# Kernel tuning notes

Measured on AMD Instinct MI355X. Metric: run time of the kernel, lower is better.

## Reference

```python
import jax, jax.numpy as jnp
import numpy as np

N, L, S, D, H = 4, 8192, 8192, 256, 8
DH = D // H  # 32
EPS_ATTN = 1e-6
EPS_LN = 1e-5


def setup_inputs() -> dict:
    key = jax.random.key(0)
    ks = jax.random.split(key, 8)
    w = lambda k, sh: jax.random.normal(k, sh, jnp.float32) * 0.02
    return {
        "x": jax.random.normal(ks[0], (N, L, D), jnp.float32),
        "source": jax.random.normal(ks[1], (N, S, D), jnp.float32),
        "Wq": w(ks[2], (D, D)),
        "Wk": w(ks[3], (D, D)),
        "Wv": w(ks[4], (D, D)),
        "Wm": w(ks[5], (D, D)),
        "W1": w(ks[6], (2 * D, 2 * D)),
        "W2": w(ks[7], (2 * D, D)),
        "g1": jnp.ones((D,), jnp.float32),
        "b1": jnp.zeros((D,), jnp.float32),
        "g2": jnp.ones((D,), jnp.float32),
        "b2": jnp.zeros((D,), jnp.float32),
    }


def _layernorm(x, g, b):
    m = jnp.mean(x, axis=-1, keepdims=True)
    v = jnp.var(x, axis=-1, keepdims=True)
    return (x - m) * jax.lax.rsqrt(v + EPS_LN) * g + b


def reference(x, source, Wq, Wk, Wv, Wm, W1, W2, g1, b1, g2, b2):
    bs = x.shape[0]
    # QKV projections (bias=False), split heads -> [N, L/S, H, DH]
    q = (x @ Wq).reshape(bs, -1, H, DH)
    k = (source @ Wk).reshape(bs, -1, H, DH)
    v = (source @ Wv).reshape(bs, -1, H, DH)
    # elu+1 feature map (linear attention, LoFTR-style)
    Q = jax.nn.elu(q) + 1.0
    K = jax.nn.elu(k) + 1.0
    v_len = v.shape[1]
    vals = v / v_len
    KV = jnp.einsum("nshd,nshv->nhdv", K, vals)  # [N, H, DH, DH]
    Z = 1.0 / (jnp.einsum("nlhd,nhd->nlh", Q, K.sum(axis=1)) + EPS_ATTN)
    msg = jnp.einsum("nlhd,nhdv,nlh->nlhv", Q, KV, Z) * v_len  # [N, L, H, DH]
    # merge heads + LN
    msg = msg.reshape(bs, -1, H * DH) @ Wm
    msg = _layernorm(msg, g1, b1)
    # concat-MLP with LeakyReLU(0.1)
    h = jnp.concatenate([x, msg], axis=2) @ W1
    h = jnp.where(h >= 0, h, 0.1 * h)
    msg = h @ W2
    msg = _layernorm(msg, g2, b2)
    return x + msg
```

## Files before the change

kernel.cpp:

```cpp
#include <hip/hip_runtime.h>

typedef __bf16 bf16;
typedef __bf16 bf16x4 __attribute__((ext_vector_type(4)));
typedef __bf16 bf16x8 __attribute__((ext_vector_type(8)));
typedef float f32x4 __attribute__((ext_vector_type(4)));

#define BM 128
#define BN 128
#define BK 64

__device__ __forceinline__ float apply_epi(float v, int epi) {
  if (epi == 1) return v > 0.f ? v + 1.f : __expf(v);
  if (epi == 2) return v >= 0.f ? v : 0.1f * v;
  return v;
}

__device__ __forceinline__ void g2l16(const bf16* gp, bf16* lp) {
  __builtin_amdgcn_global_load_lds(
      (const __attribute__((address_space(1))) void*)gp,
      (__attribute__((address_space(3))) void*)lp, 16, 0, 0);
}

__global__ void detect_kernel(const unsigned* g1raw, int* flag) {
  if (threadIdx.x == 0 && blockIdx.x == 0)
    *flag = (g1raw[0] == 0x3F800000u) ? 1 : 0;
}

struct TransArgs {
  const void* src[6];
  bf16* dst[6];
  int R[6], C[6], t0[6];
};

__global__ __launch_bounds__(256) void prep_kernel(
    const void* __restrict__ xin, const void* __restrict__ sin,
    bf16* __restrict__ bx, bf16* __restrict__ bs,
    TransArgs ta, const int* flagp) {
  const bool f32 = (*flagp != 0);
  if (blockIdx.x < 8192) {
    const void* s;
    bf16* d;
    size_t i;
    if (blockIdx.x < 4096) {
      s = xin; d = bx; i = (size_t)blockIdx.x * 2048 + threadIdx.x * 8;
    } else {
      s = sin; d = bs; i = (size_t)(blockIdx.x - 4096) * 2048 + threadIdx.x * 8;
    }
    if (f32) {
      f32x4 lo = *(const f32x4*)((const float*)s + i);
      f32x4 hi = *(const f32x4*)((const float*)s + i + 4);
      bf16x8 t;
      t[0] = (bf16)lo[0]; t[1] = (bf16)lo[1]; t[2] = (bf16)lo[2]; t[3] = (bf16)lo[3];
      t[4] = (bf16)hi[0]; t[5] = (bf16)hi[1]; t[6] = (bf16)hi[2]; t[7] = (bf16)hi[3];
      *(bf16x8*)(d + i) = t;
    } else {
      *(bf16x8*)(d + i) = *(const bf16x8*)((const bf16*)s + i);
    }
    return;
  }
  __shared__ bf16 tile[32][33];
  int bid = blockIdx.x - 8192;
  int si = 0;
#pragma unroll
  for (int i = 1; i < 6; ++i)
    if (bid >= ta.t0[i]) si = i;
  const void* srcv = ta.src[si];
  bf16* dst = ta.dst[si];
  int R = ta.R[si], Cc = ta.C[si];
  int lt = bid - ta.t0[si];
  int tpr = Cc >> 5;
  int tr = lt / tpr, tc = lt % tpr;
  int tx = threadIdx.x & 31, ty0 = threadIdx.x >> 5;
#pragma unroll
  for (int i = 0; i < 4; ++i) {
    int ty = ty0 + i * 8;
    size_t idx = (size_t)(tr * 32 + ty) * Cc + tc * 32 + tx;
    tile[ty][tx] = f32 ? (bf16)((const float*)srcv)[idx] : ((const bf16*)srcv)[idx];
  }
  __syncthreads();
#pragma unroll
  for (int i = 0; i < 4; ++i) {
    int ty = ty0 + i * 8;
    dst[(size_t)(tc * 32 + ty) * R + tr * 32 + tx] = tile[tx][ty];
  }
}

__global__ __launch_bounds__(256) void gemm_rt(
    const bf16* __restrict__ A, const bf16* __restrict__ A2, int ldA,
    const bf16* __restrict__ Bt, bf16* __restrict__ C, int Nn, int Kk, int epi,
    bf16* __restrict__ C2, int epi2, int split) {
  __shared__ bf16 As[BM * BK];
  __shared__ bf16 Bs[BN * BK];
  const int tid = threadIdx.x;
  const int m0 = blockIdx.x * BM;
  const int n0 = blockIdx.y * BN;
  const int wave = tid >> 6, lane = tid & 63;
  const int wm = (wave & 1) * 64, wn = (wave >> 1) * 64;
  const int q = lane >> 4, mr = lane & 15;

  f32x4 acc[4][4];
#pragma unroll
  for (int i = 0; i < 4; ++i)
#pragma unroll
    for (int j = 0; j < 4; ++j) acc[i][j] = (f32x4){0.f, 0.f, 0.f, 0.f};

  const int kTiles = Kk / BK;
  for (int kt = 0; kt < kTiles; ++kt) {
    int kk = kt * BK;
    const bf16* Ab = A;
    int kcol = kk;
    if (A2 && kk >= 256) { Ab = A2; kcol = kk - 256; }
    __syncthreads();
#pragma unroll
    for (int it = 0; it < 4; ++it) {
      int id = it * 256 + tid;
      int rr = id >> 3, pp = id & 7, gg = pp ^ (rr & 7);
      g2l16(Ab + (size_t)(m0 + rr) * ldA + kcol + gg * 8, &As[id * 8]);
    }
#pragma unroll
    for (int it = 0; it < 4; ++it) {
      int id = it * 256 + tid;
      int rr = id >> 3, pp = id & 7, gg = pp ^ (rr & 7);
      g2l16(Bt + (size_t)(n0 + rr) * Kk + kk + gg * 8, &Bs[id * 8]);
    }
    __syncthreads();
#pragma unroll
    for (int ks = 0; ks < 2; ++ks) {
      bf16x8 af[4], bfv[4];
#pragma unroll
      for (int mi = 0; mi < 4; ++mi) {
        int rrow = wm + mi * 16 + mr;
        af[mi] = *(const bf16x8*)&As[rrow * BK + ((ks * 4 + q) ^ (rrow & 7)) * 8];
      }
#pragma unroll
      for (int ni = 0; ni < 4; ++ni) {
        int rrow = wn + ni * 16 + mr;
        bfv[ni] = *(const bf16x8*)&Bs[rrow * BK + ((ks * 4 + q) ^ (rrow & 7)) * 8];
      }
#pragma unroll
      for (int mi = 0; mi < 4; ++mi)
#pragma unroll
        for (int ni = 0; ni < 4; ++ni)
          acc[mi][ni] = __builtin_amdgcn_mfma_f32_16x16x32_bf16(af[mi], bfv[ni], acc[mi][ni], 0, 0, 0);
    }
  }

  bf16* Cw = C;
  int nbase = n0, ep = epi;
  if (C2 && n0 >= split) { Cw = C2; nbase = n0 - split; ep = epi2; }
#pragma unroll
  for (int mi = 0; mi < 4; ++mi)
#pragma unroll
    for (int ni = 0; ni < 4; ++ni)
#pragma unroll
      for (int r4 = 0; r4 < 4; ++r4) {
        int row = m0 + wm + mi * 16 + q * 4 + r4;
        int cn = nbase + wn + ni * 16 + mr;
        float v = apply_epi(acc[mi][ni][r4], ep);
        Cw[(size_t)row * Nn + cn] = (bf16)v;
      }
}

#define KVCH 256
__global__ __launch_bounds__(256) void kv_kernel(
    const bf16* __restrict__ Kf, const bf16* __restrict__ V,
    float* __restrict__ partial, float* __restrict__ pk) {
  __shared__ bf16 Ks[KVCH][32];
  __shared__ bf16 Vs[KVCH][32];
  const int cb = blockIdx.x, h = blockIdx.y, n = blockIdx.z;
  const int tid = threadIdx.x;
  const int wave = tid >> 6, lane = tid & 63;
  const int d0 = (lane & 7) * 4, dv0 = (lane >> 3) * 4;
  const int s0 = cb * KVCH;
#pragma unroll
  for (int rd = 0; rd < 4; ++rd) {
    int rr = rd * 64 + (tid >> 2), pp = tid & 3;
    size_t g = ((size_t)(n * 8192 + s0 + rr)) * 256 + h * 32 + pp * 8;
    *(bf16x8*)&Ks[rr][pp * 8] = *(const bf16x8*)(Kf + g);
    *(bf16x8*)&Vs[rr][pp * 8] = *(const bf16x8*)(V + g);
  }
  __syncthreads();
  float acc[4][4] = {};
  float ks4[4] = {};
#pragma unroll 4
  for (int si = 0; si < 64; ++si) {
    int s = wave * 64 + si;
    bf16x4 k4 = *(const bf16x4*)&Ks[s][d0];
    bf16x4 v4 = *(const bf16x4*)&Vs[s][dv0];
    float kf[4] = {(float)k4[0], (float)k4[1], (float)k4[2], (float)k4[3]};
    float vf[4] = {(float)v4[0], (float)v4[1], (float)v4[2], (float)v4[3]};
#pragma unroll
    for (int vi = 0; vi < 4; ++vi)
#pragma unroll
      for (int di = 0; di < 4; ++di) acc[vi][di] = fmaf(vf[vi], kf[di], acc[vi][di]);
#pragma unroll
    for (int di = 0; di < 4; ++di) ks4[di] += kf[di];
  }
  __syncthreads();
  float* red = (float*)&Ks[0][0];
  float* ksr = (float*)&Vs[0][0];
#pragma unroll
  for (int vi = 0; vi < 4; ++vi)
#pragma unroll
    for (int di = 0; di < 4; ++di)
      red[wave * 1024 + (dv0 + vi) * 32 + d0 + di] = acc[vi][di];
  if (dv0 == 0) {
#pragma unroll
    for (int di = 0; di < 4; ++di) ksr[wave * 32 + d0 + di] = ks4[di];
  }
  __syncthreads();
  const size_t slot = (size_t)(n * 8 + h) * 32 + cb;
  f32x4 s4 = {0.f, 0.f, 0.f, 0.f};
#pragma unroll
  for (int w = 0; w < 4; ++w) s4 += *(const f32x4*)&red[w * 1024 + tid * 4];
  *(f32x4*)&partial[slot * 1024 + tid * 4] = s4;
  if (tid < 32) {
    float ss = 0.f;
#pragma unroll
    for (int w = 0; w < 4; ++w) ss += ksr[w * 32 + tid];
    pk[slot * 32 + tid] = ss;
  }
}

__global__ __launch_bounds__(256) void kv_reduce(
    const float* __restrict__ partial, const float* __restrict__ pk,
    float* __restrict__ kv_acc, float* __restrict__ ksum) {
  const int b = blockIdx.x;
  const int t = threadIdx.x;
  f32x4 s4 = {0.f, 0.f, 0.f, 0.f};
  for (int c = 0; c < 32; ++c)
    s4 += *(const f32x4*)&partial[((size_t)b * 32 + c) * 1024 + t * 4];
  *(f32x4*)&kv_acc[(size_t)b * 1024 + t * 4] = s4;
  if (t < 32) {
    float ss = 0.f;
    for (int c = 0; c < 32; ++c) ss += pk[((size_t)b * 32 + c) * 32 + t];
    ksum[(size_t)b * 32 + t] = ss;
  }
}

__global__ __launch_bounds__(256) void msg_kernel(
    const bf16* __restrict__ Q, const float* __restrict__ kv_acc,
    const float* __restrict__ ksum, bf16* __restrict__ msg) {
  __shared__ bf16 kvt[8][32][32];
  __shared__ float ksl[8][32];
  __shared__ float zl[8][128];
  int tid = threadIdx.x;
  int row0 = blockIdx.x * 128;
  int n = row0 >> 13;
  const float* kvb = kv_acc + (size_t)n * 8192;
  for (int i = tid; i < 8192; i += 256) ((bf16*)kvt)[i] = (bf16)kvb[i];
  ((float*)ksl)[tid] = ksum[(size_t)n * 256 + tid];
  __syncthreads();
  int r = tid & 127, hg = tid >> 7;
  const bf16* qrow = Q + (size_t)(row0 + r) * 256;
#pragma unroll
  for (int hh = 0; hh < 4; ++hh) {
    int h = hg * 4 + hh;
    float dot = 0.f;
#pragma unroll
    for (int d = 0; d < 32; ++d) dot = fmaf((float)qrow[h * 32 + d], ksl[h][d], dot);
    zl[h][r] = 1.f / (dot + 1e-6f);
  }
  __syncthreads();
  int wave = tid >> 6, lane = tid & 63, q = lane >> 4, mr = lane & 15;
  f32x4 zero = {0.f, 0.f, 0.f, 0.f};
  for (int h = 0; h < 8; ++h) {
    bf16x8 b0 = *(const bf16x8*)&kvt[h][mr][q * 8];
    bf16x8 b1 = *(const bf16x8*)&kvt[h][16 + mr][q * 8];
#pragma unroll
    for (int mi = 0; mi < 2; ++mi) {
      int arow = wave * 32 + mi * 16 + mr;
      bf16x8 a = *(const bf16x8*)(Q + (size_t)(row0 + arow) * 256 + h * 32 + q * 8);
      f32x4 c0 = __builtin_amdgcn_mfma_f32_16x16x32_bf16(a, b0, zero, 0, 0, 0);
      f32x4 c1 = __builtin_amdgcn_mfma_f32_16x16x32_bf16(a, b1, zero, 0, 0, 0);
#pragma unroll
      for (int r4 = 0; r4 < 4; ++r4) {
        int orow = wave * 32 + mi * 16 + q * 4 + r4;
        float z = zl[h][orow];
        size_t ob = (size_t)(row0 + orow) * 256 + h * 32;
        msg[ob + mr] = (bf16)(c0[r4] * z);
        msg[ob + 16 + mr] = (bf16)(c1[r4] * z);
      }
    }
  }
}

__global__ __launch_bounds__(256) void ln_kernel(
    const bf16* __restrict__ in, const void* __restrict__ g, const void* __restrict__ b,
    const void* __restrict__ resid, void* __restrict__ outp,
    const int* flagp, int ioDual) {
  const bool gbF32 = (*flagp != 0);
  const bool ioF32 = ioDual && gbF32;
  int wave = threadIdx.x >> 6, lane = threadIdx.x & 63;
  size_t row = (size_t)blockIdx.x * 4 + wave;
  int c = lane * 4;
  bf16x4 v = *(const bf16x4*)(in + row * 256 + c);
  float x0 = (float)v[0], x1 = (float)v[1], x2 = (float)v[2], x3 = (float)v[3];
  float s = x0 + x1 + x2 + x3;
  float sq = x0 * x0 + x1 * x1 + x2 * x2 + x3 * x3;
#pragma unroll
  for (int o = 32; o > 0; o >>= 1) {
    s += __shfl_xor(s, o);
    sq += __shfl_xor(sq, o);
  }
  float mean = s * (1.f / 256.f);
  float var = sq * (1.f / 256.f) - mean * mean;
  float rstd = rsqrtf(var + 1e-5f);
  float g0, g1v, g2v, g3, b0, b1v, b2v, b3;
  if (gbF32) {
    f32x4 gv = *(const f32x4*)((const float*)g + c);
    f32x4 bv = *(const f32x4*)((const float*)b + c);
    g0 = gv[0]; g1v = gv[1]; g2v = gv[2]; g3 = gv[3];
    b0 = bv[0]; b1v = bv[1]; b2v = bv[2]; b3 = bv[3];
  } else {
    bf16x4 gv = *(const bf16x4*)((const bf16*)g + c);
    bf16x4 bv = *(const bf16x4*)((const bf16*)b + c);
    g0 = (float)gv[0]; g1v = (float)gv[1]; g2v = (float)gv[2]; g3 = (float)gv[3];
    b0 = (float)bv[0]; b1v = (float)bv[1]; b2v = (float)bv[2]; b3 = (float)bv[3];
  }
  float y0 = (x0 - mean) * rstd * g0 + b0;
  float y1 = (x1 - mean) * rstd * g1v + b1v;
  float y2 = (x2 - mean) * rstd * g2v + b2v;
  float y3 = (x3 - mean) * rstd * g3 + b3;
  if (resid) {
    if (ioF32) {
      f32x4 rv = *(const f32x4*)((const float*)resid + row * 256 + c);
      y0 += rv[0]; y1 += rv[1]; y2 += rv[2]; y3 += rv[3];
    } else {
      bf16x4 rv = *(const bf16x4*)((const bf16*)resid + row * 256 + c);
      y0 += (float)rv[0]; y1 += (float)rv[1]; y2 += (float)rv[2]; y3 += (float)rv[3];
    }
  }
  if (ioF32) {
    f32x4 o4 = {y0, y1, y2, y3};
    *(f32x4*)((float*)outp + row * 256 + c) = o4;
  } else {
    bf16x4 o4;
    o4[0] = (bf16)y0; o4[1] = (bf16)y1; o4[2] = (bf16)y2; o4[3] = (bf16)y3;
    *(bf16x4*)((bf16*)outp + row * 256 + c) = o4;
  }
}

extern "C" void kernel_launch(void* const* d_in, const int* in_sizes, int n_in,
                              void* d_out, int out_size, void* d_ws, size_t ws_size,
                              hipStream_t stream) {
  const void* x   = d_in[0];
  const void* src = d_in[1];
  const void* Wq  = d_in[2];
  const void* Wk  = d_in[3];
  const void* Wv  = d_in[4];
  const void* Wm  = d_in[5];
  const void* W1  = d_in[6];
  const void* W2  = d_in[7];
  const void* g1  = d_in[8];
  const void* b1  = d_in[9];
  const void* g2  = d_in[10];
  const void* b2  = d_in[11];

  char* ws = (char*)d_ws;
  bf16* bufA = (bf16*)(ws);
  bf16* bufB = (bf16*)(ws + ((size_t)16 << 20));
  bf16* bufC = (bf16*)(ws + ((size_t)32 << 20));
  bf16* WqT  = (bf16*)(ws + ((size_t)48 << 20));
  bf16* WkvT = WqT + 65536;
  bf16* WmT  = WkvT + 131072;
  bf16* W1T  = WmT + 65536;
  bf16* W2T  = W1T + 262144;
  float* kv_acc = (float*)(ws + ((size_t)50 << 20));
  float* ksum = kv_acc + 32768;
  int* flagp = (int*)(ws + ((size_t)50 << 20) + 160 * 1024);
  float* partial = (float*)(ws + ((size_t)51 << 20));
  float* pk = (float*)(ws + ((size_t)55 << 20));
  bf16* bufX = (bf16*)d_out;
  bf16* bufS = bufX + 8388608;

  detect_kernel<<<dim3(1), dim3(64), 0, stream>>>((const unsigned*)g1, flagp);

  TransArgs ta;
  ta.src[0] = Wq; ta.src[1] = Wk; ta.src[2] = Wv; ta.src[3] = Wm; ta.src[4] = W1; ta.src[5] = W2;
  ta.dst[0] = WqT; ta.dst[1] = WkvT; ta.dst[2] = WkvT + 65536; ta.dst[3] = WmT; ta.dst[4] = W1T; ta.dst[5] = W2T;
  ta.R[0] = 256; ta.R[1] = 256; ta.R[2] = 256; ta.R[3] = 256; ta.R[4] = 512; ta.R[5] = 512;
  ta.C[0] = 256; ta.C[1] = 256; ta.C[2] = 256; ta.C[3] = 256; ta.C[4] = 512; ta.C[5] = 256;
  ta.t0[0] = 0; ta.t0[1] = 64; ta.t0[2] = 128; ta.t0[3] = 192; ta.t0[4] = 256; ta.t0[5] = 512;
  prep_kernel<<<dim3(8832), dim3(256), 0, stream>>>(x, src, bufX, bufS, ta, flagp);

  gemm_rt<<<dim3(256, 2), dim3(256), 0, stream>>>(bufX, nullptr, 256, WqT, bufA, 256, 256, 1,
                                                  nullptr, 0, 0);
  gemm_rt<<<dim3(256, 4), dim3(256), 0, stream>>>(bufS, nullptr, 256, WkvT, bufB, 256, 256, 1,
                                                  bufC, 0, 256);

  kv_kernel<<<dim3(32, 8, 4), dim3(256), 0, stream>>>(bufB, bufC, partial, pk);
  kv_reduce<<<dim3(32), dim3(256), 0, stream>>>(partial, pk, kv_acc, ksum);

  msg_kernel<<<dim3(256), dim3(256), 0, stream>>>(bufA, kv_acc, ksum, bufB);

  gemm_rt<<<dim3(256, 2), dim3(256), 0, stream>>>(bufB, nullptr, 256, WmT, bufA, 256, 256, 0,
                                                  nullptr, 0, 0);

  ln_kernel<<<dim3(8192), dim3(256), 0, stream>>>(bufA, g1, b1, nullptr, bufC, flagp, 0);

  gemm_rt<<<dim3(256, 4), dim3(256), 0, stream>>>(bufX, bufC, 256, W1T, bufA, 512, 512, 2,
                                                  nullptr, 0, 0);

  gemm_rt<<<dim3(256, 2), dim3(256), 0, stream>>>(bufA, nullptr, 512, W2T, bufC, 256, 512, 0,
                                                  nullptr, 0, 0);

  ln_kernel<<<dim3(8192), dim3(256), 0, stream>>>(bufC, g2, b2, x, d_out, flagp, 1);
}
```

Measured before the change: 284.4 us.

## Replace GEMM with double-buffered 256x256 tile kernel and swizzled block order

The 128x128 single-buffered GEMM becomes a 256x256-tile kernel with 512 threads and double-buffered LDS. The next K tile is prefetched while MFMA runs on the current one, and a block-index swizzle changes how tiles are assigned. This is meant to hide global-load latency and raise data reuse per block. In exchange the grids shrink to 128 or 256 workgroups, so occupancy on the GPU drops. The larger register footprint (32 accumulators per lane) could cause spills, and LDS use per block grows to 128 KB.

Result: slower. 293.4 us (+3.2%).

```diff
diff --git a/kernel.cpp b/kernel.cpp
--- a/kernel.cpp
+++ b/kernel.cpp
@@ -4,10 +4,6 @@
 typedef __bf16 bf16x4 __attribute__((ext_vector_type(4)));
 typedef __bf16 bf16x8 __attribute__((ext_vector_type(8)));
 typedef float f32x4 __attribute__((ext_vector_type(4)));
-
-#define BM 128
-#define BN 128
-#define BK 64
 
 __device__ __forceinline__ float apply_epi(float v, int epi) {
   if (epi == 1) return v > 0.f ? v + 1.f : __expf(v);
@@ -85,71 +81,97 @@
   }
 }
 
-__global__ __launch_bounds__(256) void gemm_rt(
+#define TM 256
+#define TN 256
+#define TK 64
+
+__device__ __forceinline__ void stage_tile(
+    const bf16* __restrict__ Ab, int ldA, int m0, int kcol,
+    const bf16* __restrict__ Bt, int Kk, int n0, int kk,
+    bf16* As, bf16* Bs, int tid) {
+#pragma unroll
+  for (int it = 0; it < 4; ++it) {
+    int id = it * 512 + tid;
+    int rr = id >> 3, pp = id & 7, gg = pp ^ (rr & 7);
+    g2l16(Ab + (size_t)(m0 + rr) * ldA + kcol + gg * 8, As + id * 8);
+  }
+#pragma unroll
+  for (int it = 0; it < 4; ++it) {
+    int id = it * 512 + tid;
+    int rr = id >> 3, pp = id & 7, gg = pp ^ (rr & 7);
+    g2l16(Bt + (size_t)(n0 + rr) * Kk + kk + gg * 8, Bs + id * 8);
+  }
+}
+
+__global__ __launch_bounds__(512, 2) void gemm256(
     const bf16* __restrict__ A, const bf16* __restrict__ A2, int ldA,
     const bf16* __restrict__ Bt, bf16* __restrict__ C, int Nn, int Kk, int epi,
-    bf16* __restrict__ C2, int epi2, int split) {
-  __shared__ bf16 As[BM * BK];
-  __shared__ bf16 Bs[BN * BK];
+    bf16* __restrict__ C2, int epi2, int split, int gridM) {
+  __shared__ bf16 As[2][TM * TK];
+  __shared__ bf16 Bs[2][TN * TK];
   const int tid = threadIdx.x;
-  const int m0 = blockIdx.x * BM;
-  const int n0 = blockIdx.y * BN;
+
+  const int nwg = gridDim.x;
+  const int cpx = nwg >> 3;
+  const int swz = (blockIdx.x & 7) * cpx + (blockIdx.x >> 3);
+  const int mb = swz % gridM, nb = swz / gridM;
+  const int m0 = mb * TM, n0 = nb * TN;
+
   const int wave = tid >> 6, lane = tid & 63;
-  const int wm = (wave & 1) * 64, wn = (wave >> 1) * 64;
+  const int wm = (wave >> 2) * 128, wn = (wave & 3) * 64;
   const int q = lane >> 4, mr = lane & 15;
 
-  f32x4 acc[4][4];
-#pragma unroll
-  for (int i = 0; i < 4; ++i)
+  f32x4 acc[8][4];
+#pragma unroll
+  for (int i = 0; i < 8; ++i)
 #pragma unroll
     for (int j = 0; j < 4; ++j) acc[i][j] = (f32x4){0.f, 0.f, 0.f, 0.f};
 
-  const int kTiles = Kk / BK;
+  const int kTiles = Kk / TK;
+
+  stage_tile(A, ldA, m0, 0, Bt, Kk, n0, 0, As[0], Bs[0], tid);
+
   for (int kt = 0; kt < kTiles; ++kt) {
-    int kk = kt * BK;
-    const bf16* Ab = A;
-    int kcol = kk;
-    if (A2 && kk >= 256) { Ab = A2; kcol = kk - 256; }
-    __syncthreads();
-#pragma unroll
-    for (int it = 0; it < 4; ++it) {
-      int id = it * 256 + tid;
-      int rr = id >> 3, pp = id & 7, gg = pp ^ (rr & 7);
-      g2l16(Ab + (size_t)(m0 + rr) * ldA + kcol + gg * 8, &As[id * 8]);
-    }
-#pragma unroll
-    for (int it = 0; it < 4; ++it) {
-      int id = it * 256 + tid;
-      int rr = id >> 3, pp = id & 7, gg = pp ^ (rr & 7);
-      g2l16(Bt + (size_t)(n0 + rr) * Kk + kk + gg * 8, &Bs[id * 8]);
-    }
-    __syncthreads();
+    const int nxt = kt + 1;
+    if (nxt < kTiles) {
+      int kk = nxt * TK;
+      const bf16* Ab = A;
+      int kcol = kk;
+      if (A2 && kk >= 256) { Ab = A2; kcol = kk - 256; }
+      stage_tile(Ab, ldA, m0, kcol, Bt, Kk, n0, kk, As[nxt & 1], Bs[nxt & 1], tid);
+      asm volatile("s_waitcnt vmcnt(8)\n\ts_barrier" ::: "memory");
+    } else {
+      asm volatile("s_waitcnt vmcnt(0)\n\ts_barrier" ::: "memory");
+    }
+    const bf16* Asb = As[kt & 1];
+    const bf16* Bsb = Bs[kt & 1];
 #pragma unroll
     for (int ks = 0; ks < 2; ++ks) {
-      bf16x8 af[4], bfv[4];
-#pragma unroll
-      for (int mi = 0; mi < 4; ++mi) {
+      bf16x8 af[8], bfv[4];
+#pragma unroll
+      for (int mi = 0; mi < 8; ++mi) {
         int rrow = wm + mi * 16 + mr;
-        af[mi] = *(const bf16x8*)&As[rrow * BK + ((ks * 4 + q) ^ (rrow & 7)) * 8];
+        af[mi] = *(const bf16x8*)&Asb[rrow * TK + ((ks * 4 + q) ^ (rrow & 7)) * 8];
       }
 #pragma unroll
       for (int ni = 0; ni < 4; ++ni) {
         int rrow = wn + ni * 16 + mr;
-        bfv[ni] = *(const bf16x8*)&Bs[rrow * BK + ((ks * 4 + q) ^ (rrow & 7)) * 8];
+        bfv[ni] = *(const bf16x8*)&Bsb[rrow * TK + ((ks * 4 + q) ^ (rrow & 7)) * 8];
       }
 #pragma unroll
-      for (int mi = 0; mi < 4; ++mi)
+      for (int mi = 0; mi < 8; ++mi)
 #pragma unroll
         for (int ni = 0; ni < 4; ++ni)
           acc[mi][ni] = __builtin_amdgcn_mfma_f32_16x16x32_bf16(af[mi], bfv[ni], acc[mi][ni], 0, 0, 0);
     }
+    asm volatile("s_waitcnt lgkmcnt(0)\n\ts_barrier" ::: "memory");
   }
 
   bf16* Cw = C;
   int nbase = n0, ep = epi;
   if (C2 && n0 >= split) { Cw = C2; nbase = n0 - split; ep = epi2; }
 #pragma unroll
-  for (int mi = 0; mi < 4; ++mi)
+  for (int mi = 0; mi < 8; ++mi)
 #pragma unroll
     for (int ni = 0; ni < 4; ++ni)
 #pragma unroll
@@ -384,26 +406,26 @@
   ta.t0[0] = 0; ta.t0[1] = 64; ta.t0[2] = 128; ta.t0[3] = 192; ta.t0[4] = 256; ta.t0[5] = 512;
   prep_kernel<<<dim3(8832), dim3(256), 0, stream>>>(x, src, bufX, bufS, ta, flagp);
 
-  gemm_rt<<<dim3(256, 2), dim3(256), 0, stream>>>(bufX, nullptr, 256, WqT, bufA, 256, 256, 1,
-                                                  nullptr, 0, 0);
-  gemm_rt<<<dim3(256, 4), dim3(256), 0, stream>>>(bufS, nullptr, 256, WkvT, bufB, 256, 256, 1,
-                                                  bufC, 0, 256);
+  gemm256<<<dim3(128), dim3(512), 0, stream>>>(bufX, nullptr, 256, WqT, bufA, 256, 256, 1,
+                                               nullptr, 0, 0, 128);
+  gemm256<<<dim3(256), dim3(512), 0, stream>>>(bufS, nullptr, 256, WkvT, bufB, 256, 256, 1,
+                                               bufC, 0, 256, 128);
 
   kv_kernel<<<dim3(32, 8, 4), dim3(256), 0, stream>>>(bufB, bufC, partial, pk);
   kv_reduce<<<dim3(32), dim3(256), 0, stream>>>(partial, pk, kv_acc, ksum);
 
   msg_kernel<<<dim3(256), dim3(256), 0, stream>>>(bufA, kv_acc, ksum, bufB);
 
-  gemm_rt<<<dim3(256, 2), dim3(256), 0, stream>>>(bufB, nullptr, 256, WmT, bufA, 256, 256, 0,
-                                                  nullptr, 0, 0);
+  gemm256<<<dim3(128), dim3(512), 0, stream>>>(bufB, nullptr, 256, WmT, bufA, 256, 256, 0,
+                                               nullptr, 0, 0, 128);
 
   ln_kernel<<<dim3(8192), dim3(256), 0, stream>>>(bufA, g1, b1, nullptr, bufC, flagp, 0);
 
-  gemm_rt<<<dim3(256, 4), dim3(256), 0, stream>>>(bufX, bufC, 256, W1T, bufA, 512, 512, 2,
-                                                  nullptr, 0, 0);
-
-  gemm_rt<<<dim3(256, 2), dim3(256), 0, stream>>>(bufA, nullptr, 512, W2T, bufC, 256, 512, 0,
-                                                  nullptr, 0, 0);
+  gemm256<<<dim3(256), dim3(512), 0, stream>>>(bufX, bufC, 256, W1T, bufA, 512, 512, 2,
+                                               nullptr, 0, 0, 128);
+
+  gemm256<<<dim3(128), dim3(512), 0, stream>>>(bufA, nullptr, 512, W2T, bufC, 256, 512, 0,
+                                               nullptr, 0, 0, 128);
 
   ln_kernel<<<dim3(8192), dim3(256), 0, stream>>>(bufC, g2, b2, x, d_out, flagp, 1);
 }
```
